# Performance work log

Hardware: AMD Instinct MI355X
Metric: run time of the kernel (lower is better)

## Reference

```python
import jax, jax.numpy as jnp
import numpy as np

EPS = 1e-10


def setup_inputs() -> dict:
    key = jax.random.key(0)
    k1, k2, k3 = jax.random.split(key, 3)
    B, X, Y = 16, 512, 512
    predictions = jax.random.uniform(k1, (B, 5, X, Y), dtype=jnp.float32)
    inputs = jax.random.uniform(k2, (B, 3, X, Y), dtype=jnp.float32)
    heart = jax.random.randint(k3, (B, 1, X, Y), 0, 2, dtype=jnp.int32)
    return {"predictions": predictions, "inputs": inputs, "heart": heart}


def reference(predictions, inputs, heart):
    # predictions: [B,5,X,Y] soft class maps (chan 0 unused); inputs: [B,3,X,Y] MRI modalities
    # heart: [B,1,X,Y] binary ROI mask. Loops over b/k/m in the torch source are vectorized;
    # boolean-mask gathers become multiply-by-mask with masked reductions (same math).
    mask = (heart[:, 0] == 1).astype(predictions.dtype)          # [B,X,Y]
    pred = predictions[:, 1:5]                                   # [B,K=4,X,Y]
    inp = inputs                                                 # [B,M=3,X,Y]

    w = pred * mask[:, None]                                     # masked soft weights [B,K,X,Y]
    sw = jnp.sum(w, axis=(2, 3))                                 # [B,K]
    denom = sw[:, :, None] + EPS                                 # [B,K,1]

    # per-(k,m) weighted mean over masked pixels
    mu = jnp.einsum('bkxy,bmxy->bkm', w, inp) / denom            # [B,K,M]
    diff = inp[:, None, :, :, :] - mu[:, :, :, None, None]       # [B,K,M,X,Y]
    var = jnp.einsum('bkxy,bkmxy->bkm', w, diff * diff) / denom + EPS

    # Gaussian pdf per (k,m,pixel), scaled by pred_k (as in temp[k,m] = pred[k]*pdf)
    inv_norm = 1.0 / jnp.sqrt(2.0 * jnp.pi * var)                # [B,K,M]
    pdf = inv_norm[:, :, :, None, None] * jnp.exp(
        -(diff * diff) / (2.0 * var)[:, :, :, None, None])      # [B,K,M,X,Y]
    temp = pred[:, :, None] * pdf                                # [B,K,M,X,Y]

    mix = jnp.sum(jnp.prod(temp, axis=2), axis=1)                # [B,X,Y]
    loglik = jnp.log(mix + EPS)                                  # [B,X,Y]

    # masked mean over ROI pixels per batch (== torch.mean over gathered pixels)
    per_b = -jnp.sum(loglik * mask, axis=(1, 2)) / jnp.sum(mask, axis=(1, 2))
    return jnp.mean(per_b)
```

## Files before the change

kernel.cpp:

```cpp
#include <hip/hip_runtime.h>
#include <math.h>

constexpr int NB = 16;
constexpr int XY = 512 * 512;
constexpr int NV = XY / 4;
constexpr int GRIDX = 128;
constexpr int BLK = 256;
constexpr int WS_STRIDE = 32;


__device__ __forceinline__ float waveReduce64(float v) {
#pragma unroll
    for (int off = 32; off > 0; off >>= 1) v += __shfl_down(v, off, 64);
    return v;
}

#define PIX1(h_, e0_, e1_, e2_, p0_, p1_, p2_, p3_) do {                      \
    float mm_ = ((h_) == 1) ? 1.f : 0.f;                                      \
    cnt += mm_;                                                               \
    float w0_ = (p0_) * mm_, w1_ = (p1_) * mm_, w2_ = (p2_) * mm_,            \
          w3_ = (p3_) * mm_;                                                  \
    s0_0 += w0_; s0_1 += w1_; s0_2 += w2_; s0_3 += w3_;                       \
    float t_;                                                                 \
    t_ = w0_ * (e0_); u00 += t_; q00 = fmaf(t_, (e0_), q00);                  \
    t_ = w0_ * (e1_); u01 += t_; q01 = fmaf(t_, (e1_), q01);                  \
    t_ = w0_ * (e2_); u02 += t_; q02 = fmaf(t_, (e2_), q02);                  \
    t_ = w1_ * (e0_); u10 += t_; q10 = fmaf(t_, (e0_), q10);                  \
    t_ = w1_ * (e1_); u11 += t_; q11 = fmaf(t_, (e1_), q11);                  \
    t_ = w1_ * (e2_); u12 += t_; q12 = fmaf(t_, (e2_), q12);                  \
    t_ = w2_ * (e0_); u20 += t_; q20 = fmaf(t_, (e0_), q20);                  \
    t_ = w2_ * (e1_); u21 += t_; q21 = fmaf(t_, (e1_), q21);                  \
    t_ = w2_ * (e2_); u22 += t_; q22 = fmaf(t_, (e2_), q22);                  \
    t_ = w3_ * (e0_); u30 += t_; q30 = fmaf(t_, (e0_), q30);                  \
    t_ = w3_ * (e1_); u31 += t_; q31 = fmaf(t_, (e1_), q31);                  \
    t_ = w3_ * (e2_); u32 += t_; q32 = fmaf(t_, (e2_), q32);                  \
} while (0)

#define RED(i_, var_) { float r_ = waveReduce64(var_); if (lane == 0) sh[wav][i_] = r_; }

__global__ __launch_bounds__(256) void pass1_moments(
        const float* __restrict__ predictions,
        const float* __restrict__ inputs,
        const int*   __restrict__ heart,
        double*      __restrict__ ws) {
    const int b = blockIdx.y;
    const float4* P1 = reinterpret_cast<const float4*>(predictions + (size_t)b * 5 * XY + 1 * XY);
    const float4* P2 = reinterpret_cast<const float4*>(predictions + (size_t)b * 5 * XY + 2 * XY);
    const float4* P3 = reinterpret_cast<const float4*>(predictions + (size_t)b * 5 * XY + 3 * XY);
    const float4* P4 = reinterpret_cast<const float4*>(predictions + (size_t)b * 5 * XY + 4 * XY);
    const float4* I0 = reinterpret_cast<const float4*>(inputs + (size_t)b * 3 * XY + 0 * XY);
    const float4* I1 = reinterpret_cast<const float4*>(inputs + (size_t)b * 3 * XY + 1 * XY);
    const float4* I2 = reinterpret_cast<const float4*>(inputs + (size_t)b * 3 * XY + 2 * XY);
    const int4*   H  = reinterpret_cast<const int4*>(heart + (size_t)b * XY);

    float cnt = 0.f;
    float s0_0 = 0.f, s0_1 = 0.f, s0_2 = 0.f, s0_3 = 0.f;
    float u00 = 0.f, u01 = 0.f, u02 = 0.f, u10 = 0.f, u11 = 0.f, u12 = 0.f;
    float u20 = 0.f, u21 = 0.f, u22 = 0.f, u30 = 0.f, u31 = 0.f, u32 = 0.f;
    float q00 = 0.f, q01 = 0.f, q02 = 0.f, q10 = 0.f, q11 = 0.f, q12 = 0.f;
    float q20 = 0.f, q21 = 0.f, q22 = 0.f, q30 = 0.f, q31 = 0.f, q32 = 0.f;

    const int tid0   = blockIdx.x * BLK + threadIdx.x;
    const int stride = GRIDX * BLK;

    for (int v = tid0; v < NV; v += stride) {
        int4   h  = H[v];
        float4 f0 = I0[v], f1 = I1[v], f2 = I2[v];
        float4 g0 = P1[v], g1 = P2[v], g2 = P3[v], g3 = P4[v];
        PIX1(h.x, f0.x, f1.x, f2.x, g0.x, g1.x, g2.x, g3.x);
        PIX1(h.y, f0.y, f1.y, f2.y, g0.y, g1.y, g2.y, g3.y);
        PIX1(h.z, f0.z, f1.z, f2.z, g0.z, g1.z, g2.z, g3.z);
        PIX1(h.w, f0.w, f1.w, f2.w, g0.w, g1.w, g2.w, g3.w);
    }

    __shared__ float sh[4][29];
    const int lane = threadIdx.x & 63;
    const int wav  = threadIdx.x >> 6;
    RED(0, cnt);
    RED(1, s0_0); RED(2, s0_1); RED(3, s0_2); RED(4, s0_3);
    RED(5, u00); RED(6, u01); RED(7, u02);
    RED(8, u10); RED(9, u11); RED(10, u12);
    RED(11, u20); RED(12, u21); RED(13, u22);
    RED(14, u30); RED(15, u31); RED(16, u32);
    RED(17, q00); RED(18, q01); RED(19, q02);
    RED(20, q10); RED(21, q11); RED(22, q12);
    RED(23, q20); RED(24, q21); RED(25, q22);
    RED(26, q30); RED(27, q31); RED(28, q32);
    __syncthreads();
    if (threadIdx.x < 29) {
        float v = sh[0][threadIdx.x] + sh[1][threadIdx.x] + sh[2][threadIdx.x] + sh[3][threadIdx.x];
        atomicAdd(&ws[(size_t)b * WS_STRIDE + threadIdx.x], (double)v);
    }
}

#define PARAMK(K_, mu0_, mu1_, mu2_, h0_, h1_, h2_, C_) {                     \
    double S0_ = w[1 + (K_)];                                                 \
    double den_ = S0_ + 1e-10;                                                \
    double Cd_ = 1.0;                                                         \
    double S1_, S2_, muv_, var_;                                              \
    S1_ = w[5 + (K_)*3 + 0]; S2_ = w[17 + (K_)*3 + 0];                        \
    muv_ = S1_ / den_;                                                        \
    var_ = (S2_ - 2.0 * muv_ * S1_ + muv_ * muv_ * S0_) / den_ + 1e-10;       \
    mu0_ = (float)muv_; h0_ = (float)(0.5 / var_);                            \
    Cd_ *= 1.0 / sqrt(6.283185307179586 * var_);                              \
    S1_ = w[5 + (K_)*3 + 1]; S2_ = w[17 + (K_)*3 + 1];                        \
    muv_ = S1_ / den_;                                                        \
    var_ = (S2_ - 2.0 * muv_ * S1_ + muv_ * muv_ * S0_) / den_ + 1e-10;       \
    mu1_ = (float)muv_; h1_ = (float)(0.5 / var_);                            \
    Cd_ *= 1.0 / sqrt(6.283185307179586 * var_);                              \
    S1_ = w[5 + (K_)*3 + 2]; S2_ = w[17 + (K_)*3 + 2];                        \
    muv_ = S1_ / den_;                                                        \
    var_ = (S2_ - 2.0 * muv_ * S1_ + muv_ * muv_ * S0_) / den_ + 1e-10;       \
    mu2_ = (float)muv_; h2_ = (float)(0.5 / var_);                            \
    Cd_ *= 1.0 / sqrt(6.283185307179586 * var_);                              \
    C_ = (float)Cd_;                                                          \
}

#define PIX2(h_, e0_, e1_, e2_, p0_, p1_, p2_, p3_) do {                      \
    float m_ = ((h_) == 1) ? 1.f : 0.f;                                       \
    float d0_, d1_, d2_, ex_, pc_;                                            \
    float mix_;                                                               \
    d0_ = (e0_) - mu00; d1_ = (e1_) - mu01; d2_ = (e2_) - mu02;               \
    ex_ = fmaf(d0_ * d0_, hv00, fmaf(d1_ * d1_, hv01, d2_ * d2_ * hv02));     \
    pc_ = (p0_) * (p0_) * (p0_);                                              \
    mix_ = C0 * pc_ * __expf(-ex_);                                           \
    d0_ = (e0_) - mu10; d1_ = (e1_) - mu11; d2_ = (e2_) - mu12;               \
    ex_ = fmaf(d0_ * d0_, hv10, fmaf(d1_ * d1_, hv11, d2_ * d2_ * hv12));     \
    pc_ = (p1_) * (p1_) * (p1_);                                              \
    mix_ = fmaf(C1 * pc_, __expf(-ex_), mix_);                                \
    d0_ = (e0_) - mu20; d1_ = (e1_) - mu21; d2_ = (e2_) - mu22;               \
    ex_ = fmaf(d0_ * d0_, hv20, fmaf(d1_ * d1_, hv21, d2_ * d2_ * hv22));     \
    pc_ = (p2_) * (p2_) * (p2_);                                              \
    mix_ = fmaf(C2 * pc_, __expf(-ex_), mix_);                                \
    d0_ = (e0_) - mu30; d1_ = (e1_) - mu31; d2_ = (e2_) - mu32;               \
    ex_ = fmaf(d0_ * d0_, hv30, fmaf(d1_ * d1_, hv31, d2_ * d2_ * hv32));     \
    pc_ = (p3_) * (p3_) * (p3_);                                              \
    mix_ = fmaf(C3 * pc_, __expf(-ex_), mix_);                                \
    lacc += m_ * __logf(mix_ + 1e-10f);                                       \
} while (0)

__global__ __launch_bounds__(256) void pass2_loglik(
        const float* __restrict__ predictions,
        const float* __restrict__ inputs,
        const int*   __restrict__ heart,
        double*      __restrict__ ws) {
    const int b = blockIdx.y;
    const double* w = ws + (size_t)b * WS_STRIDE;

    float mu00, mu01, mu02, mu10, mu11, mu12, mu20, mu21, mu22, mu30, mu31, mu32;
    float hv00, hv01, hv02, hv10, hv11, hv12, hv20, hv21, hv22, hv30, hv31, hv32;
    float C0, C1, C2, C3;
    PARAMK(0, mu00, mu01, mu02, hv00, hv01, hv02, C0);
    PARAMK(1, mu10, mu11, mu12, hv10, hv11, hv12, C1);
    PARAMK(2, mu20, mu21, mu22, hv20, hv21, hv22, C2);
    PARAMK(3, mu30, mu31, mu32, hv30, hv31, hv32, C3);

    const float4* P1 = reinterpret_cast<const float4*>(predictions + (size_t)b * 5 * XY + 1 * XY);
    const float4* P2 = reinterpret_cast<const float4*>(predictions + (size_t)b * 5 * XY + 2 * XY);
    const float4* P3 = reinterpret_cast<const float4*>(predictions + (size_t)b * 5 * XY + 3 * XY);
    const float4* P4 = reinterpret_cast<const float4*>(predictions + (size_t)b * 5 * XY + 4 * XY);
    const float4* I0 = reinterpret_cast<const float4*>(inputs + (size_t)b * 3 * XY + 0 * XY);
    const float4* I1 = reinterpret_cast<const float4*>(inputs + (size_t)b * 3 * XY + 1 * XY);
    const float4* I2 = reinterpret_cast<const float4*>(inputs + (size_t)b * 3 * XY + 2 * XY);
    const int4*   H  = reinterpret_cast<const int4*>(heart + (size_t)b * XY);

    float lacc = 0.f;
    const int tid0   = blockIdx.x * BLK + threadIdx.x;
    const int stride = GRIDX * BLK;

    for (int v = tid0; v < NV; v += stride) {
        int4   h  = H[v];
        float4 f0 = I0[v], f1 = I1[v], f2 = I2[v];
        float4 g0 = P1[v], g1 = P2[v], g2 = P3[v], g3 = P4[v];
        PIX2(h.x, f0.x, f1.x, f2.x, g0.x, g1.x, g2.x, g3.x);
        PIX2(h.y, f0.y, f1.y, f2.y, g0.y, g1.y, g2.y, g3.y);
        PIX2(h.z, f0.z, f1.z, f2.z, g0.z, g1.z, g2.z, g3.z);
        PIX2(h.w, f0.w, f1.w, f2.w, g0.w, g1.w, g2.w, g3.w);
    }

    __shared__ float sh[4];
    const int lane = threadIdx.x & 63;
    const int wav  = threadIdx.x >> 6;
    float v = waveReduce64(lacc);
    if (lane == 0) sh[wav] = v;
    __syncthreads();
    if (threadIdx.x == 0) {
        float t = sh[0] + sh[1] + sh[2] + sh[3];
        atomicAdd(&ws[(size_t)b * WS_STRIDE + 29], (double)t);
    }
}

__global__ void finalize_kernel(const double* __restrict__ ws, float* __restrict__ out) {
    const int lane = threadIdx.x;
    double v = 0.0;
    if (lane < NB) {
        double cntv = ws[(size_t)lane * WS_STRIDE + 0];
        double ll   = ws[(size_t)lane * WS_STRIDE + 29];
        v = -ll / cntv;
    }
#pragma unroll
    for (int off = 8; off > 0; off >>= 1) v += __shfl_down(v, off, 64);
    if (lane == 0) out[0] = (float)(v / (double)NB);
}

extern "C" void kernel_launch(void* const* d_in, const int* in_sizes, int n_in,
                              void* d_out, int out_size, void* d_ws, size_t ws_size,
                              hipStream_t stream) {
    const float* predictions = (const float*)d_in[0];
    const float* inputs      = (const float*)d_in[1];
    const int*   heart       = (const int*)d_in[2];
    float*  out = (float*)d_out;
    double* ws  = (double*)d_ws;

    hipMemsetAsync(d_ws, 0, (size_t)NB * WS_STRIDE * sizeof(double), stream);

    pass1_moments<<<dim3(GRIDX, NB), BLK, 0, stream>>>(predictions, inputs, heart, ws);
    pass2_loglik <<<dim3(GRIDX, NB), BLK, 0, stream>>>(predictions, inputs, heart, ws);
    finalize_kernel<<<1, 64, 0, stream>>>(ws, out);
}
```

Before: 198.0 us.

## Stage per-tile channel loads into LDS via global_load_lds and halve grid

Both passes now load each 256-vector tile of all eight channel planes into shared memory, using the async global-to-LDS load builtin when it is available, then compute from LDS. Each block walks a contiguous range of tiles, and the grid is halved to 64 blocks per batch. The aim is to turn eight strided per-thread global loads into wave-wide direct-to-LDS transfers. The cost is a single-buffered tile with two barriers per iteration and no prefetch, so load latency is not overlapped with compute, and there are fewer blocks to hide that latency.

```diff
diff --git a/kernel.cpp b/kernel.cpp
--- a/kernel.cpp
+++ b/kernel.cpp
@@ -4,8 +4,11 @@
 constexpr int NB = 16;
 constexpr int XY = 512 * 512;
 constexpr int NV = XY / 4;
-constexpr int GRIDX = 128;
 constexpr int BLK = 256;
+constexpr int GRIDX = 64;
+constexpr int TILE_V = 256;
+constexpr int TILES_PER_BATCH = NV / TILE_V;
+constexpr int TPB = TILES_PER_BATCH / GRIDX;
 constexpr int WS_STRIDE = 32;
 
 
@@ -14,6 +17,17 @@
     for (int off = 32; off > 0; off >>= 1) v += __shfl_down(v, off, 64);
     return v;
 }
+
+#if __has_builtin(__builtin_amdgcn_global_load_lds)
+#define HAVE_GLL 1
+__device__ __forceinline__ void g2lds16(const void* g, void* l) {
+    __builtin_amdgcn_global_load_lds(
+        (const __attribute__((address_space(1))) void*)g,
+        (__attribute__((address_space(3))) void*)l, 16, 0, 0);
+}
+#else
+#define HAVE_GLL 0
+#endif
 
 #define PIX1(h_, e0_, e1_, e2_, p0_, p1_, p2_, p3_) do {                      \
     float mm_ = ((h_) == 1) ? 1.f : 0.f;                                      \
@@ -38,20 +52,47 @@
 
 #define RED(i_, var_) { float r_ = waveReduce64(var_); if (lane == 0) sh[wav][i_] = r_; }
 
+#define STAGE_TILE(tile_)                                                     \
+    {                                                                         \
+        const int vbase_ = (tile_) * TILE_V;                                  \
+        _Pragma("unroll")                                                     \
+        for (int jj_ = 0; jj_ < 8; ++jj_) {                                   \
+            int j_ = wav * 8 + jj_;                                           \
+            int ch_ = j_ >> 2, chunk_ = j_ & 3;                               \
+            const float4* gp_ = cb[ch_] + (vbase_ + chunk_ * 64 + lane);      \
+            STAGE_ONE(gp_, ch_, chunk_);                                      \
+        }                                                                     \
+    }
+
+#if HAVE_GLL
+#define STAGE_ONE(gp_, ch_, chunk_) g2lds16((const void*)(gp_), (void*)&tileBuf[ch_][(chunk_) * 64])
+#else
+#define STAGE_ONE(gp_, ch_, chunk_) tileBuf[ch_][(chunk_) * 64 + lane] = *(gp_)
+#endif
+
 __global__ __launch_bounds__(256) void pass1_moments(
         const float* __restrict__ predictions,
         const float* __restrict__ inputs,
         const int*   __restrict__ heart,
         double*      __restrict__ ws) {
     const int b = blockIdx.y;
-    const float4* P1 = reinterpret_cast<const float4*>(predictions + (size_t)b * 5 * XY + 1 * XY);
-    const float4* P2 = reinterpret_cast<const float4*>(predictions + (size_t)b * 5 * XY + 2 * XY);
-    const float4* P3 = reinterpret_cast<const float4*>(predictions + (size_t)b * 5 * XY + 3 * XY);
-    const float4* P4 = reinterpret_cast<const float4*>(predictions + (size_t)b * 5 * XY + 4 * XY);
-    const float4* I0 = reinterpret_cast<const float4*>(inputs + (size_t)b * 3 * XY + 0 * XY);
-    const float4* I1 = reinterpret_cast<const float4*>(inputs + (size_t)b * 3 * XY + 1 * XY);
-    const float4* I2 = reinterpret_cast<const float4*>(inputs + (size_t)b * 3 * XY + 2 * XY);
-    const int4*   H  = reinterpret_cast<const int4*>(heart + (size_t)b * XY);
+
+    __shared__ float4 tileBuf[8][TILE_V];
+    __shared__ const float4* cb[8];
+    __shared__ float sh[4][29];
+
+    const int tx   = threadIdx.x;
+    const int lane = tx & 63;
+    const int wav  = tx >> 6;
+
+    if (tx < 8) {
+        const float* p;
+        if (tx == 0)      p = (const float*)(heart + (size_t)b * XY);
+        else if (tx <= 3) p = inputs + (size_t)b * 3 * XY + (size_t)(tx - 1) * XY;
+        else              p = predictions + (size_t)b * 5 * XY + (size_t)(tx - 3) * XY;
+        cb[tx] = reinterpret_cast<const float4*>(p);
+    }
+    __syncthreads();
 
     float cnt = 0.f;
     float s0_0 = 0.f, s0_1 = 0.f, s0_2 = 0.f, s0_3 = 0.f;
@@ -60,22 +101,20 @@
     float q00 = 0.f, q01 = 0.f, q02 = 0.f, q10 = 0.f, q11 = 0.f, q12 = 0.f;
     float q20 = 0.f, q21 = 0.f, q22 = 0.f, q30 = 0.f, q31 = 0.f, q32 = 0.f;
 
-    const int tid0   = blockIdx.x * BLK + threadIdx.x;
-    const int stride = GRIDX * BLK;
-
-    for (int v = tid0; v < NV; v += stride) {
-        int4   h  = H[v];
-        float4 f0 = I0[v], f1 = I1[v], f2 = I2[v];
-        float4 g0 = P1[v], g1 = P2[v], g2 = P3[v], g3 = P4[v];
+    const int tile0 = blockIdx.x * TPB;
+    for (int t = 0; t < TPB; ++t) {
+        STAGE_TILE(tile0 + t);
+        __syncthreads();
+        int4   h  = ((const int4*)tileBuf[0])[tx];
+        float4 f0 = tileBuf[1][tx], f1 = tileBuf[2][tx], f2 = tileBuf[3][tx];
+        float4 g0 = tileBuf[4][tx], g1 = tileBuf[5][tx], g2 = tileBuf[6][tx], g3 = tileBuf[7][tx];
         PIX1(h.x, f0.x, f1.x, f2.x, g0.x, g1.x, g2.x, g3.x);
         PIX1(h.y, f0.y, f1.y, f2.y, g0.y, g1.y, g2.y, g3.y);
         PIX1(h.z, f0.z, f1.z, f2.z, g0.z, g1.z, g2.z, g3.z);
         PIX1(h.w, f0.w, f1.w, f2.w, g0.w, g1.w, g2.w, g3.w);
-    }
-
-    __shared__ float sh[4][29];
-    const int lane = threadIdx.x & 63;
-    const int wav  = threadIdx.x >> 6;
+        __syncthreads();
+    }
+
     RED(0, cnt);
     RED(1, s0_0); RED(2, s0_1); RED(3, s0_2); RED(4, s0_3);
     RED(5, u00); RED(6, u01); RED(7, u02);
@@ -87,9 +126,9 @@
     RED(23, q20); RED(24, q21); RED(25, q22);
     RED(26, q30); RED(27, q31); RED(28, q32);
     __syncthreads();
-    if (threadIdx.x < 29) {
-        float v = sh[0][threadIdx.x] + sh[1][threadIdx.x] + sh[2][threadIdx.x] + sh[3][threadIdx.x];
-        atomicAdd(&ws[(size_t)b * WS_STRIDE + threadIdx.x], (double)v);
+    if (tx < 29) {
+        float v = sh[0][tx] + sh[1][tx] + sh[2][tx] + sh[3][tx];
+        atomicAdd(&ws[(size_t)b * WS_STRIDE + tx], (double)v);
     }
 }
 
@@ -155,38 +194,44 @@
     PARAMK(2, mu20, mu21, mu22, hv20, hv21, hv22, C2);
     PARAMK(3, mu30, mu31, mu32, hv30, hv31, hv32, C3);
 
-    const float4* P1 = reinterpret_cast<const float4*>(predictions + (size_t)b * 5 * XY + 1 * XY);
-    const float4* P2 = reinterpret_cast<const float4*>(predictions + (size_t)b * 5 * XY + 2 * XY);
-    const float4* P3 = reinterpret_cast<const float4*>(predictions + (size_t)b * 5 * XY + 3 * XY);
-    const float4* P4 = reinterpret_cast<const float4*>(predictions + (size_t)b * 5 * XY + 4 * XY);
-    const float4* I0 = reinterpret_cast<const float4*>(inputs + (size_t)b * 3 * XY + 0 * XY);
-    const float4* I1 = reinterpret_cast<const float4*>(inputs + (size_t)b * 3 * XY + 1 * XY);
-    const float4* I2 = reinterpret_cast<const float4*>(inputs + (size_t)b * 3 * XY + 2 * XY);
-    const int4*   H  = reinterpret_cast<const int4*>(heart + (size_t)b * XY);
+    __shared__ float4 tileBuf[8][TILE_V];
+    __shared__ const float4* cb[8];
+    __shared__ float sh[4];
+
+    const int tx   = threadIdx.x;
+    const int lane = tx & 63;
+    const int wav  = tx >> 6;
+
+    if (tx < 8) {
+        const float* p;
+        if (tx == 0)      p = (const float*)(heart + (size_t)b * XY);
+        else if (tx <= 3) p = inputs + (size_t)b * 3 * XY + (size_t)(tx - 1) * XY;
+        else              p = predictions + (size_t)b * 5 * XY + (size_t)(tx - 3) * XY;
+        cb[tx] = reinterpret_cast<const float4*>(p);
+    }
+    __syncthreads();
 
     float lacc = 0.f;
-    const int tid0   = blockIdx.x * BLK + threadIdx.x;
-    const int stride = GRIDX * BLK;
-
-    for (int v = tid0; v < NV; v += stride) {
-        int4   h  = H[v];
-        float4 f0 = I0[v], f1 = I1[v], f2 = I2[v];
-        float4 g0 = P1[v], g1 = P2[v], g2 = P3[v], g3 = P4[v];
+    const int tile0 = blockIdx.x * TPB;
+    for (int t = 0; t < TPB; ++t) {
+        STAGE_TILE(tile0 + t);
+        __syncthreads();
+        int4   h  = ((const int4*)tileBuf[0])[tx];
+        float4 f0 = tileBuf[1][tx], f1 = tileBuf[2][tx], f2 = tileBuf[3][tx];
+        float4 g0 = tileBuf[4][tx], g1 = tileBuf[5][tx], g2 = tileBuf[6][tx], g3 = tileBuf[7][tx];
         PIX2(h.x, f0.x, f1.x, f2.x, g0.x, g1.x, g2.x, g3.x);
         PIX2(h.y, f0.y, f1.y, f2.y, g0.y, g1.y, g2.y, g3.y);
         PIX2(h.z, f0.z, f1.z, f2.z, g0.z, g1.z, g2.z, g3.z);
         PIX2(h.w, f0.w, f1.w, f2.w, g0.w, g1.w, g2.w, g3.w);
-    }
-
-    __shared__ float sh[4];
-    const int lane = threadIdx.x & 63;
-    const int wav  = threadIdx.x >> 6;
+        __syncthreads();
+    }
+
     float v = waveReduce64(lacc);
     if (lane == 0) sh[wav] = v;
     __syncthreads();
-    if (threadIdx.x == 0) {
-        float t = sh[0] + sh[1] + sh[2] + sh[3];
-        atomicAdd(&ws[(size_t)b * WS_STRIDE + 29], (double)t);
+    if (tx == 0) {
+        float tsum = sh[0] + sh[1] + sh[2] + sh[3];
+        atomicAdd(&ws[(size_t)b * WS_STRIDE + 29], (double)tsum);
     }
 }
 
```

New measurement: 196.3 us. No clear change (-0.8%).
